# Performance work log

Measured on AMD Instinct MI355X. Metric: run time of the kernel, lower is better.

## Reference

```python
import jax, jax.numpy as jnp
import numpy as np

# Dims: B=32 batch, C=64 feat channels, Np=192 priors, No=72 row offsets,
# Ns=36 pooled sample points (maxpool kernel 2), Hd=64 fc hidden.
B, C, Np, No, Hd = 32, 64, 192, 72, 64
NS_POOL = 2  # n_offsets // sample_points
REG_DIM = No + 4  # reg_layers output


def bilinear_sample(feat, gx, gy):
    """torch F.grid_sample(align_corners=True) equivalent for in-range coords.
    feat: [B,C,H,W]; gx,gy: [B,Np,S] normalized to [-1,1]. -> [B,C,Np,S]."""
    Bb, Cc, H, W = feat.shape
    ix = (gx + 1.0) * 0.5 * (W - 1)
    iy = (gy + 1.0) * 0.5 * (H - 1)
    ix0f = jnp.floor(ix); iy0f = jnp.floor(iy)
    wx = ix - ix0f; wy = iy - iy0f
    ix0 = jnp.clip(ix0f.astype(jnp.int32), 0, W - 1)
    iy0 = jnp.clip(iy0f.astype(jnp.int32), 0, H - 1)
    ix1 = jnp.clip(ix0 + 1, 0, W - 1)
    iy1 = jnp.clip(iy0 + 1, 0, H - 1)
    ff = feat.reshape(Bb, Cc, H * W)
    S = gx.shape[1] * gx.shape[2]
    def gather(iy_, ix_):
        idx = (iy_ * W + ix_).reshape(Bb, 1, S)
        g = jnp.take_along_axis(ff, jnp.broadcast_to(idx, (Bb, Cc, S)), axis=2)
        return g.reshape(Bb, Cc, gx.shape[1], gx.shape[2])
    v00 = gather(iy0, ix0); v01 = gather(iy0, ix1)
    v10 = gather(iy1, ix0); v11 = gather(iy1, ix1)
    wx = wx[:, None]; wy = wy[:, None]  # broadcast over C
    return (v00 * (1 - wx) * (1 - wy) + v01 * wx * (1 - wy)
            + v10 * (1 - wx) * wy + v11 * wx * wy)


def _mlp2(h, Ws, bs):
    # two stacked Linear+ReLU layers (num_fc=2)
    for i in range(2):
        h = jax.nn.relu(h @ Ws[i] + bs[i])
    return h


def setup_inputs() -> dict:
    key = jax.random.key(0)
    ks = jax.random.split(key, 24)
    w = lambda k, sh: jax.random.normal(k, sh, dtype=jnp.float32) * 0.05
    return {
        "x0": jax.random.normal(ks[0], (B, C, 40, 100), dtype=jnp.float32),
        "x1": jax.random.normal(ks[1], (B, C, 20, 50), dtype=jnp.float32),
        "x2": jax.random.normal(ks[2], (B, C, 10, 25), dtype=jnp.float32),
        "prior_xs0": jax.random.uniform(ks[3], (Np, No), dtype=jnp.float32),
        "l_weight": w(ks[4], (No,)),              # self.l embedding, sigmoid gate
        "lsgi_w": w(ks[5], (3, C, C)),            # per-stage lsgi projection
        "fc_w": w(ks[6], (C, Hd)), "fc_b": w(ks[7], (Hd,)),
        "cls_w": w(ks[8], (2, Hd, Hd)), "cls_b": w(ks[9], (2, Hd)),
        "cls_ow": w(ks[10], (Hd, 2)), "cls_ob": w(ks[11], (2,)),
        "reg_w": w(ks[12], (2, Hd, Hd)), "reg_b": w(ks[13], (2, Hd)),
        "reg_ow": w(ks[14], (Hd, REG_DIM)), "reg_ob": w(ks[15], (REG_DIM,)),
        "loc_w": w(ks[16], (2, Hd, Hd)), "loc_b": w(ks[17], (2, Hd)),
        "loc_ow": w(ks[18], (Hd, 1)), "loc_ob": w(ks[19], (1,)),
    }


def reference(x0, x1, x2, prior_xs0, l_weight, lsgi_w, fc_w, fc_b,
              cls_w, cls_b, cls_ow, cls_ob, reg_w, reg_b, reg_ow, reg_ob,
              loc_w, loc_b, loc_ow, loc_ob):
    pyramid = [x2, x1, x0]  # reversed: coarsest level first (stage 0)
    prior_feat_ys = jnp.linspace(1.0, 0.0, No, dtype=jnp.float32)
    gy = jnp.broadcast_to((prior_feat_ys * 2.0 - 1.0)[None, None, :], (B, Np, No))
    prior_xs = jnp.broadcast_to(prior_xs0[None], (B, Np, No))
    gate = jax.nn.sigmoid(l_weight)[:, None]  # [No,1]
    stage_feats = []
    outs = []
    for s in range(3):
        gx = prior_xs * 2.0 - 1.0
        pooled = bilinear_sample(pyramid[s], gx, gy)          # [B,C,Np,No]
        pooled = jnp.transpose(pooled, (0, 2, 3, 1)) * gate   # [B,Np,No,C]
        pooled = jax.nn.relu(jnp.einsum('bnoc,cd->bnod', pooled, lsgi_w[s]))
        # MaxPool2d kernel (2,1) over the offset axis -> Ns=36 sample points
        comp = pooled.reshape(B, Np, No // NS_POOL, NS_POOL, C).max(axis=3)
        stage_feats.append(comp)
        # cross-stage fusion (global head): mean over stages and sample points
        fused = jnp.stack(stage_feats, 0).mean(axis=0).mean(axis=2)  # [B,Np,C]
        fc = jax.nn.relu(fused @ fc_w + fc_b)                        # [B,Np,Hd]
        cls = _mlp2(fc, cls_w, cls_b) @ cls_ow + cls_ob              # [B,Np,2]
        reg = _mlp2(fc, reg_w, reg_b) @ reg_ow + reg_ob              # [B,Np,No+4]
        loc = _mlp2(fc, loc_w, loc_b) @ loc_ow + loc_ob              # [B,Np,1]
        outs.append(jnp.concatenate([cls, reg, loc], axis=-1))      # [B,Np,79]
        # refine anchors for next stage from predicted xs
        prior_xs = jax.nn.sigmoid(reg[..., 4:])
    return jnp.stack(outs, axis=0)  # [3,B,Np,79]
```

## Files before the change

### kernel.cpp

```cpp
#include <hip/hip_runtime.h>
#include <hip/hip_bf16.h>

#define Bq   32
#define Cq   64
#define NPq  192
#define NOq  72
#define PTS  (NPq * NOq)
#define REGD 76
#define OUTD 79

typedef __attribute__((ext_vector_type(8))) short short8;
typedef __attribute__((ext_vector_type(4))) float float4v;

__device__ inline unsigned short f2bf(float x) {
    __hip_bfloat16 h = __float2bfloat16(x);
    return *reinterpret_cast<unsigned short*>(&h);
}
__device__ inline float bf2f(unsigned short u) {
    unsigned int x = ((unsigned int)u) << 16;
    float f;
    __builtin_memcpy(&f, &x, 4);
    return f;
}

template<int H, int W>
__device__ __forceinline__ void build_one(
    const float* __restrict__ feat, unsigned short* __restrict__ tab,
    const float* __restrict__ lw, const int b, const int o,
    float* __restrict__ sRow, const int tid)
{
    constexpr int Wp = W + 1;

    const float ys = 1.0f - (float)o * (1.0f / 71.0f);
    const float iy = ys * (float)(H - 1);
    const float fy = floorf(iy);
    const float wy = iy - fy;
    int iy0 = (int)fy; iy0 = iy0 < 0 ? 0 : (iy0 > H - 1 ? H - 1 : iy0);
    const int iy1 = (iy0 + 1 > H - 1) ? H - 1 : iy0 + 1;
    const float gate = 1.0f / (1.0f + __expf(-lw[o]));

    const float* fb = feat + (size_t)b * 64 * H * W;
    const int iy0W = iy0 * W, iy1W = iy1 * W;

    constexpr int tot = 64 * W;
    for (int idx = tid; idx < tot; idx += 256) {
        const int c = idx / W;
        const int x = idx - c * W;
        const float* f = fb + c * (H * W);
        sRow[c * Wp + x] = ((1.0f - wy) * f[iy0W + x] + wy * f[iy1W + x]) * gate;
    }
    __syncthreads();

    unsigned int* to = (unsigned int*)(tab + (size_t)(b * NOq + o) * Wp * 64);
    constexpr int tot2 = Wp * 32;
    for (int idx = tid; idx < tot2; idx += 256) {
        const int x  = idx >> 5;
        const int c0 = (idx & 31) * 2;
        const int xx = (x < W) ? x : (W - 1);
        const unsigned int lo = f2bf(sRow[c0 * Wp + xx]);
        const unsigned int hi = f2bf(sRow[(c0 + 1) * Wp + xx]);
        to[x * 32 + (c0 >> 1)] = lo | (hi << 16);
    }
}

__global__ __launch_bounds__(256) void build_tables_kernel(
    const float* __restrict__ f0,
    const float* __restrict__ f1,
    const float* __restrict__ f2,
    const float* __restrict__ lw,
    unsigned short* __restrict__ t0,
    unsigned short* __restrict__ t1,
    unsigned short* __restrict__ t2)
{
    __shared__ float sRow[64 * 101];
    const int tid = threadIdx.x;
    const int o   = blockIdx.x / 96;
    const int sb  = blockIdx.x - o * 96;
    const int s   = sb >> 5;
    const int b   = sb & 31;

    if (s == 0)      build_one<10, 25 >(f0, t0, lw, b, o, sRow, tid);
    else if (s == 1) build_one<20, 50 >(f1, t1, lw, b, o, sRow, tid);
    else             build_one<40, 100>(f2, t2, lw, b, o, sRow, tid);
}

template<int W>
__global__ __launch_bounds__(256) void fused_pool_head_kernel(
    const unsigned short* __restrict__ tab,
    const float* __restrict__ xsrc, const int xstride,
    const float* __restrict__ lsgi,
    float* __restrict__ sumFeat,
    const int stage,
    const float* __restrict__ fc_w,  const float* __restrict__ fc_b,
    const float* __restrict__ cls_w, const float* __restrict__ cls_b,
    const float* __restrict__ cls_ow, const float* __restrict__ cls_ob,
    const float* __restrict__ reg_w, const float* __restrict__ reg_b,
    const float* __restrict__ reg_ow, const float* __restrict__ reg_ob,
    const float* __restrict__ loc_w, const float* __restrict__ loc_b,
    const float* __restrict__ loc_ow, const float* __restrict__ loc_ob,
    float* __restrict__ out, float* __restrict__ xs_next)
{
    constexpr int Wp = W + 1;
    __shared__ __align__(16) float sF [8][68];
    __shared__ __align__(16) float sC [8][68];
    __shared__ __align__(16) float sT1[8][68];
    __shared__ __align__(16) float sT2[8][68];
    __shared__ __align__(16) float sWt[4864];

    const int tid  = threadIdx.x;
    const int w    = tid >> 6;
    const int lane = tid & 63;
    const int ng   = blockIdx.x >> 5;
    const int b    = blockIdx.x & 31;
    const int npair = ng * 4 + w;

    short8 wf[4][2];
    {
        const int kb = ((lane >> 4) & 3) * 8;
        const int dl = lane & 15;
        #pragma unroll
        for (int ks = 0; ks < 2; ++ks)
            #pragma unroll
            for (int dt = 0; dt < 4; ++dt) {
                union { unsigned short u[8]; short8 v; } pk;
                #pragma unroll
                for (int j = 0; j < 8; ++j)
                    pk.u[j] = f2bf(lsgi[(ks * 32 + kb + j) * 64 + dt * 16 + dl]);
                wf[dt][ks] = pk.v;
            }
    }

    const unsigned short* tb = tab + (size_t)b * NOq * Wp * 64;
    const float* xp = xsrc + (size_t)xstride * b;
    const int m  = lane & 15;
    const int kg = lane >> 4;
    const int nt0 = npair * 9;

    float sums0[4] = {0.f, 0.f, 0.f, 0.f};
    float sums1[4] = {0.f, 0.f, 0.f, 0.f};

    #pragma unroll
    for (int ntl = 0; ntl < 9; ++ntl) {
        const int pt = (nt0 + ntl) * 16 + m;
        const int o  = pt % NOq;
        float ixf = xp[pt] * (float)(W - 1);
        ixf = fminf(fmaxf(ixf, 0.0f), (float)(W - 1));
        const float fx = floorf(ixf);
        const float wx = ixf - fx;
        const int ix0 = (int)fx;

        const unsigned short* col = tb + ((size_t)o * Wp + ix0) * 64 + kg * 8;
        union { unsigned short u[8]; short8 v; } t00, t01, t10, t11, a0, a1;
        t00.v = *(const short8*)(col);
        t01.v = *(const short8*)(col + 64);
        t10.v = *(const short8*)(col + 32);
        t11.v = *(const short8*)(col + 96);
        #pragma unroll
        for (int j = 0; j < 8; ++j) {
            const float l0 = bf2f(t00.u[j]), h0 = bf2f(t01.u[j]);
            const float l1 = bf2f(t10.u[j]), h1 = bf2f(t11.u[j]);
            a0.u[j] = f2bf(l0 + wx * (h0 - l0));
            a1.u[j] = f2bf(l1 + wx * (h1 - l1));
        }

        const bool hi = (ntl * 16 + (kg * 4)) >= NOq;
        #pragma unroll
        for (int dt = 0; dt < 4; ++dt) {
            float4v c = {0.f, 0.f, 0.f, 0.f};
            c = __builtin_amdgcn_mfma_f32_16x16x32_bf16(a0.v, wf[dt][0], c, 0, 0, 0);
            c = __builtin_amdgcn_mfma_f32_16x16x32_bf16(a1.v, wf[dt][1], c, 0, 0, 0);
            const float pm0 = fmaxf(fmaxf(c[0], c[1]), 0.f);
            const float pm1 = fmaxf(fmaxf(c[2], c[3]), 0.f);
            const float add = pm0 + pm1;
            if (hi) sums1[dt] += add; else sums0[dt] += add;
        }
    }

    #pragma unroll
    for (int dt = 0; dt < 4; ++dt) {
        float v0 = sums0[dt], v1 = sums1[dt];
        v0 += __shfl_xor(v0, 16); v0 += __shfl_xor(v0, 32);
        v1 += __shfl_xor(v1, 16); v1 += __shfl_xor(v1, 32);
        sums0[dt] = v0; sums1[dt] = v1;
    }

    const float invS = 1.0f / (float)(stage + 1);
    if (lane < 16) {
        const size_t row0 = (size_t)(b * NPq + npair * 2) * 64;
        #pragma unroll
        for (int dt = 0; dt < 4; ++dt) {
            const int d = dt * 16 + lane;
            float t0 = sums0[dt] * (1.0f / 36.0f);
            float t1 = sums1[dt] * (1.0f / 36.0f);
            float* p0 = sumFeat + row0 + d;
            float* p1 = sumFeat + row0 + 64 + d;
            if (stage > 0) { t0 += *p0; t1 += *p1; }
            *p0 = t0; *p1 = t1;
            sF[2 * w][d]     = t0 * invS;
            sF[2 * w + 1][d] = t1 * invS;
        }
    }

    const int pt2 = tid >> 5;
    const int dh  = tid & 31;
    const int d0  = dh * 2;
    const int p0g = b * NPq + ng * 8;

    auto gemm64 = [&](const float (*src)[68], float (*dst)[68],
                      const float* __restrict__ gw, const float* __restrict__ gb) {
        __syncthreads();
        #pragma unroll
        for (int i = 0; i < 4; ++i)
            *(float4*)&sWt[(i * 256 + tid) * 4] = *(const float4*)&gw[(i * 256 + tid) * 4];
        __syncthreads();
        float a0 = gb[d0], a1 = gb[d0 + 1];
        #pragma unroll 8
        for (int k = 0; k < 64; ++k) {
            const float av = src[pt2][k];
            const float2 w2 = *(const float2*)&sWt[k * 64 + d0];
            a0 += av * w2.x; a1 += av * w2.y;
        }
        dst[pt2][d0]     = fmaxf(a0, 0.f);
        dst[pt2][d0 + 1] = fmaxf(a1, 0.f);
    };

    gemm64(sF, sC, fc_w, fc_b);

    gemm64(sC,  sT1, cls_w,        cls_b);
    gemm64(sT1, sT2, cls_w + 4096, cls_b + 64);
    __syncthreads();
    if (tid < 16) {
        const int p = tid >> 1, d = tid & 1;
        float z = cls_ob[d];
        #pragma unroll 8
        for (int k = 0; k < 64; ++k) z += sT2[p][k] * cls_ow[k * 2 + d];
        out[(size_t)(p0g + p) * OUTD + d] = z;
    }

    gemm64(sC,  sT1, reg_w,        reg_b);
    gemm64(sT1, sT2, reg_w + 4096, reg_b + 64);
    __syncthreads();
    for (int idx = tid; idx < 64 * REGD; idx += 256) sWt[idx] = reg_ow[idx];
    __syncthreads();
    {
        float* orow = out + (size_t)(p0g + pt2) * OUTD;
        float* xsp  = xs_next + (size_t)(p0g + pt2) * NOq;
        for (int j = dh; j < REGD; j += 32) {
            float z = reg_ob[j];
            #pragma unroll 8
            for (int k = 0; k < 64; ++k) z += sT2[pt2][k] * sWt[k * REGD + j];
            orow[2 + j] = z;
            if (j >= 4) xsp[j - 4] = 1.0f / (1.0f + __expf(-z));
        }
    }

    gemm64(sC,  sT1, loc_w,        loc_b);
    gemm64(sT1, sT2, loc_w + 4096, loc_b + 64);
    __syncthreads();
    if (tid < 8) {
        float z = loc_ob[0];
        #pragma unroll 8
        for (int k = 0; k < 64; ++k) z += sT2[tid][k] * loc_ow[k];
        out[(size_t)(p0g + tid) * OUTD + 78] = z;
    }
}

extern "C" void kernel_launch(void* const* d_in, const int* in_sizes, int n_in,
                              void* d_out, int out_size, void* d_ws, size_t ws_size,
                              hipStream_t stream)
{
    const float* x0        = (const float*)d_in[0];
    const float* x1        = (const float*)d_in[1];
    const float* x2        = (const float*)d_in[2];
    const float* prior_xs0 = (const float*)d_in[3];
    const float* l_weight  = (const float*)d_in[4];
    const float* lsgi_w    = (const float*)d_in[5];
    const float* fc_w      = (const float*)d_in[6];
    const float* fc_b      = (const float*)d_in[7];
    const float* cls_w     = (const float*)d_in[8];
    const float* cls_b     = (const float*)d_in[9];
    const float* cls_ow    = (const float*)d_in[10];
    const float* cls_ob    = (const float*)d_in[11];
    const float* reg_w     = (const float*)d_in[12];
    const float* reg_b     = (const float*)d_in[13];
    const float* reg_ow    = (const float*)d_in[14];
    const float* reg_ob    = (const float*)d_in[15];
    const float* loc_w     = (const float*)d_in[16];
    const float* loc_b     = (const float*)d_in[17];
    const float* loc_ow    = (const float*)d_in[18];
    const float* loc_ob    = (const float*)d_in[19];

    float* out     = (float*)d_out;
    float* sumFeat = (float*)d_ws;
    float* xs      = sumFeat + (size_t)Bq * NPq * Cq;
    unsigned short* tab0 = (unsigned short*)(xs + (size_t)Bq * PTS);
    unsigned short* tab1 = tab0 + (size_t)Bq * NOq * 26  * 64;
    unsigned short* tab2 = tab1 + (size_t)Bq * NOq * 51  * 64;

    hipLaunchKernelGGL(build_tables_kernel, dim3(3 * Bq * NOq), dim3(256), 0, stream,
                       x2, x1, x0, l_weight, tab0, tab1, tab2);

    for (int s = 0; s < 3; ++s) {
        const float* xsrc = (s == 0) ? prior_xs0 : xs;
        const int xstr    = (s == 0) ? 0 : PTS;
        const unsigned short* tb = (s == 0) ? tab0 : (s == 1) ? tab1 : tab2;
        float* outS = out + (size_t)s * Bq * NPq * OUTD;
        if (s == 0)
            hipLaunchKernelGGL((fused_pool_head_kernel<25>), dim3(Bq * 24), dim3(256), 0, stream,
                               tb, xsrc, xstr, lsgi_w + s * 4096, sumFeat, s,
                               fc_w, fc_b, cls_w, cls_b, cls_ow, cls_ob,
                               reg_w, reg_b, reg_ow, reg_ob,
                               loc_w, loc_b, loc_ow, loc_ob, outS, xs);
        else if (s == 1)
            hipLaunchKernelGGL((fused_pool_head_kernel<50>), dim3(Bq * 24), dim3(256), 0, stream,
                               tb, xsrc, xstr, lsgi_w + s * 4096, sumFeat, s,
                               fc_w, fc_b, cls_w, cls_b, cls_ow, cls_ob,
                               reg_w, reg_b, reg_ow, reg_ob,
                               loc_w, loc_b, loc_ow, loc_ob, outS, xs);
        else
            hipLaunchKernelGGL((fused_pool_head_kernel<100>), dim3(Bq * 24), dim3(256), 0, stream,
                               tb, xsrc, xstr, lsgi_w + s * 4096, sumFeat, s,
                               fc_w, fc_b, cls_w, cls_b, cls_ow, cls_ob,
                               reg_w, reg_b, reg_ow, reg_ob,
                               loc_w, loc_b, loc_ow, loc_ob, outS, xs);
    }
}
```

Measured before the change: 259.5 us.

## Move x-interpolation after MFMA projection and de-template table build

Because the lsgi projection is linear, the kernel now runs the MFMA on both the left and right bf16 columns and does the x-direction lerp on the fp32 outputs. This removes the per-element bf16 unpack, lerp and repack before the matmul, at the cost of doubling the MFMA count per tile and adding shuffles to fetch each row's wx. The table build kernel also drops its templated helper for runtime H/W and writes single bf16 values instead of packed pairs. That makes the build loops non-constant and the stores narrower.

```diff
diff --git a/kernel.cpp b/kernel.cpp
--- a/kernel.cpp
+++ b/kernel.cpp
@@ -21,46 +21,6 @@
     float f;
     __builtin_memcpy(&f, &x, 4);
     return f;
-}
-
-template<int H, int W>
-__device__ __forceinline__ void build_one(
-    const float* __restrict__ feat, unsigned short* __restrict__ tab,
-    const float* __restrict__ lw, const int b, const int o,
-    float* __restrict__ sRow, const int tid)
-{
-    constexpr int Wp = W + 1;
-
-    const float ys = 1.0f - (float)o * (1.0f / 71.0f);
-    const float iy = ys * (float)(H - 1);
-    const float fy = floorf(iy);
-    const float wy = iy - fy;
-    int iy0 = (int)fy; iy0 = iy0 < 0 ? 0 : (iy0 > H - 1 ? H - 1 : iy0);
-    const int iy1 = (iy0 + 1 > H - 1) ? H - 1 : iy0 + 1;
-    const float gate = 1.0f / (1.0f + __expf(-lw[o]));
-
-    const float* fb = feat + (size_t)b * 64 * H * W;
-    const int iy0W = iy0 * W, iy1W = iy1 * W;
-
-    constexpr int tot = 64 * W;
-    for (int idx = tid; idx < tot; idx += 256) {
-        const int c = idx / W;
-        const int x = idx - c * W;
-        const float* f = fb + c * (H * W);
-        sRow[c * Wp + x] = ((1.0f - wy) * f[iy0W + x] + wy * f[iy1W + x]) * gate;
-    }
-    __syncthreads();
-
-    unsigned int* to = (unsigned int*)(tab + (size_t)(b * NOq + o) * Wp * 64);
-    constexpr int tot2 = Wp * 32;
-    for (int idx = tid; idx < tot2; idx += 256) {
-        const int x  = idx >> 5;
-        const int c0 = (idx & 31) * 2;
-        const int xx = (x < W) ? x : (W - 1);
-        const unsigned int lo = f2bf(sRow[c0 * Wp + xx]);
-        const unsigned int hi = f2bf(sRow[(c0 + 1) * Wp + xx]);
-        to[x * 32 + (c0 >> 1)] = lo | (hi << 16);
-    }
 }
 
 __global__ __launch_bounds__(256) void build_tables_kernel(
@@ -73,15 +33,47 @@
     unsigned short* __restrict__ t2)
 {
     __shared__ float sRow[64 * 101];
+
     const int tid = threadIdx.x;
     const int o   = blockIdx.x / 96;
     const int sb  = blockIdx.x - o * 96;
     const int s   = sb >> 5;
     const int b   = sb & 31;
 
-    if (s == 0)      build_one<10, 25 >(f0, t0, lw, b, o, sRow, tid);
-    else if (s == 1) build_one<20, 50 >(f1, t1, lw, b, o, sRow, tid);
-    else             build_one<40, 100>(f2, t2, lw, b, o, sRow, tid);
+    const float* feat; unsigned short* tab; int H, W;
+    if (s == 0)      { feat = f0; tab = t0; H = 10; W = 25; }
+    else if (s == 1) { feat = f1; tab = t1; H = 20; W = 50; }
+    else             { feat = f2; tab = t2; H = 40; W = 100; }
+    const int Wp = W + 1;
+
+    const float ys = 1.0f - (float)o * (1.0f / 71.0f);
+    const float iy = ys * (float)(H - 1);
+    const float fy = floorf(iy);
+    const float wy = iy - fy;
+    int iy0 = (int)fy; iy0 = iy0 < 0 ? 0 : (iy0 > H - 1 ? H - 1 : iy0);
+    const int iy1 = (iy0 + 1 > H - 1) ? H - 1 : iy0 + 1;
+    const float gate = 1.0f / (1.0f + __expf(-lw[o]));
+
+    const float* fb = feat + (size_t)b * 64 * H * W;
+    const int iy0W = iy0 * W, iy1W = iy1 * W;
+
+    const int tot = 64 * W;
+    for (int idx = tid; idx < tot; idx += 256) {
+        const int c = idx / W;
+        const int x = idx - c * W;
+        const float* f = fb + c * (H * W);
+        sRow[c * Wp + x] = ((1.0f - wy) * f[iy0W + x] + wy * f[iy1W + x]) * gate;
+    }
+    __syncthreads();
+
+    unsigned short* to = tab + (size_t)(b * NOq + o) * Wp * 64;
+    const int tot2 = Wp * 64;
+    for (int idx = tid; idx < tot2; idx += 256) {
+        const int x = idx >> 6;
+        const int c = idx & 63;
+        const int xx = (x < W) ? x : (W - 1);
+        to[idx] = f2bf(sRow[c * Wp + xx]);
+    }
 }
 
 template<int W>
@@ -150,27 +142,30 @@
         const int ix0 = (int)fx;
 
         const unsigned short* col = tb + ((size_t)o * Wp + ix0) * 64 + kg * 8;
-        union { unsigned short u[8]; short8 v; } t00, t01, t10, t11, a0, a1;
-        t00.v = *(const short8*)(col);
-        t01.v = *(const short8*)(col + 64);
-        t10.v = *(const short8*)(col + 32);
-        t11.v = *(const short8*)(col + 96);
-        #pragma unroll
-        for (int j = 0; j < 8; ++j) {
-            const float l0 = bf2f(t00.u[j]), h0 = bf2f(t01.u[j]);
-            const float l1 = bf2f(t10.u[j]), h1 = bf2f(t11.u[j]);
-            a0.u[j] = f2bf(l0 + wx * (h0 - l0));
-            a1.u[j] = f2bf(l1 + wx * (h1 - l1));
-        }
+        const short8 a00 = *(const short8*)(col);
+        const short8 a01 = *(const short8*)(col + 64);
+        const short8 a10 = *(const short8*)(col + 32);
+        const short8 a11 = *(const short8*)(col + 96);
+
+        float wxr[4];
+        #pragma unroll
+        for (int j = 0; j < 4; ++j) wxr[j] = __shfl(wx, kg * 4 + j);
 
         const bool hi = (ntl * 16 + (kg * 4)) >= NOq;
         #pragma unroll
         for (int dt = 0; dt < 4; ++dt) {
-            float4v c = {0.f, 0.f, 0.f, 0.f};
-            c = __builtin_amdgcn_mfma_f32_16x16x32_bf16(a0.v, wf[dt][0], c, 0, 0, 0);
-            c = __builtin_amdgcn_mfma_f32_16x16x32_bf16(a1.v, wf[dt][1], c, 0, 0, 0);
-            const float pm0 = fmaxf(fmaxf(c[0], c[1]), 0.f);
-            const float pm1 = fmaxf(fmaxf(c[2], c[3]), 0.f);
+            float4v c0 = {0.f, 0.f, 0.f, 0.f};
+            float4v c1 = {0.f, 0.f, 0.f, 0.f};
+            c0 = __builtin_amdgcn_mfma_f32_16x16x32_bf16(a00, wf[dt][0], c0, 0, 0, 0);
+            c0 = __builtin_amdgcn_mfma_f32_16x16x32_bf16(a10, wf[dt][1], c0, 0, 0, 0);
+            c1 = __builtin_amdgcn_mfma_f32_16x16x32_bf16(a01, wf[dt][0], c1, 0, 0, 0);
+            c1 = __builtin_amdgcn_mfma_f32_16x16x32_bf16(a11, wf[dt][1], c1, 0, 0, 0);
+            const float v0 = c0[0] + wxr[0] * (c1[0] - c0[0]);
+            const float v1 = c0[1] + wxr[1] * (c1[1] - c0[1]);
+            const float v2 = c0[2] + wxr[2] * (c1[2] - c0[2]);
+            const float v3 = c0[3] + wxr[3] * (c1[3] - c0[3]);
+            const float pm0 = fmaxf(fmaxf(v0, v1), 0.f);
+            const float pm1 = fmaxf(fmaxf(v2, v3), 0.f);
             const float add = pm0 + pm1;
             if (hi) sums1[dt] += add; else sums0[dt] += add;
         }
```

New measurement: 249.7 us. 3.8% less time.
